# Performance work log

Hardware: AMD Instinct MI355X
Metric: run time of the kernel (lower is better)

## Reference

```python
import jax, jax.numpy as jnp
import numpy as np

B, S, H = 4, 256, 768
NUM_BASIC = 4
NUM_REL = 32            # labels 1..31 are real edges, 0 = no edge
NUM_ALL = 2 * NUM_REL   # bidir: forward slots 0..31, reverse slots 33..63


def setup_inputs() -> dict:
    key = jax.random.key(0)
    k1, k2, k3, k4, k5 = jax.random.split(key, 5)
    hidden_states = jax.random.normal(k1, (B, S, H), dtype=jnp.float32)
    rels = jax.random.randint(k2, (B, S, S), 0, NUM_REL, dtype=jnp.int32)
    # xavier-ish init scale for params
    basic_matrix = jax.random.normal(k3, (NUM_BASIC, H, H), dtype=jnp.float32) * 0.02
    rel_weight = jax.random.normal(k4, (NUM_ALL, NUM_BASIC), dtype=jnp.float32) * 0.1
    self_weight = jax.random.normal(k5, (H, H), dtype=jnp.float32) * 0.02  # Linear weight (out,in)
    return {"hidden_states": hidden_states, "rels": rels,
            "basic_matrix": basic_matrix, "rel_weight": rel_weight,
            "self_weight": self_weight}


def reference(hidden_states, rels, basic_matrix, rel_weight, self_weight):
    dt = hidden_states.dtype
    # forward-direction one-hot relation tensor [B, NUM_ALL, S, S], masked where rels == 0
    fwd_mask = (rels > 0).astype(dt)                                   # [B,S,S]
    fwd_oh = jax.nn.one_hot(rels, NUM_ALL, axis=1, dtype=dt) * fwd_mask[:, None]
    # reverse direction (bidir): labels shifted by NUM_REL, zeroed where no edge
    rev_rels_raw = jnp.transpose(rels, (0, 2, 1))
    rev_rels = jnp.where(rev_rels_raw > 0, rev_rels_raw + NUM_REL, 0)  # {0} U {33..63}
    rev_mask = (rev_rels > 0).astype(dt)
    rev_oh = jax.nn.one_hot(rev_rels, NUM_ALL, axis=1, dtype=dt) * rev_mask[:, None]
    rel_tensor = fwd_oh + rev_oh                                       # [B,R,S,S]

    # basis decomposition: per-relation transform [R, H, H]
    rel_matrix = jnp.einsum('rb,bio->rio', rel_weight, basic_matrix)
    # per-relation transformed hidden states [B,R,S,H]
    r_hidden = jnp.einsum('bsi,rio->brso', hidden_states, rel_matrix)
    # adjacency aggregation [B,R,S,H]
    r_ctx = jnp.einsum('brij,brjo->brio', rel_tensor, r_hidden)
    # mean over neighbors (clamp count at 1)
    num_neighbors = jnp.maximum(rel_tensor.sum(-1), 1.0)               # [B,R,S]
    r_ctx = r_ctx / num_neighbors[..., None]
    context = r_ctx.sum(axis=1)                                        # [B,S,H]
    self_layer = hidden_states @ self_weight.T
    return self_layer + context
```

## Files before the change

### kernel.cpp

```cpp
#include <hip/hip_runtime.h>
#include <stdint.h>

typedef unsigned short u16;
typedef unsigned int u32;
typedef __attribute__((ext_vector_type(8))) short short8;
typedef __attribute__((ext_vector_type(4))) float float4v;

#define Bb 4
#define Ss 256
#define Hh 768
#define NALL 64


__device__ __forceinline__ float b2f(u16 h) {
    u32 u = ((u32)h) << 16;
    float f;
    __builtin_memcpy(&f, &u, 4);
    return f;
}
__device__ __forceinline__ u16 f2b(float f) {
    u32 u;
    __builtin_memcpy(&u, &f, 4);
    u = (u + 0x7fffu + ((u >> 16) & 1u)) >> 16;
    return (u16)u;
}

__global__ __launch_bounds__(256) void k_prep(const float* __restrict__ h,
                                              const int* __restrict__ rels,
                                              const float* __restrict__ basic,
                                              const float* __restrict__ relw,
                                              const float* __restrict__ selfw,
                                              u16* __restrict__ basicT,
                                              u16* __restrict__ coefC,
                                              u16* __restrict__ hbf,
                                              u16* __restrict__ swbf) {
    __shared__ u16 tile[32][34];
    __shared__ float srelw[256];
    __shared__ u32 hist[NALL];
    const int z = blockIdx.x;
    const int t = threadIdx.x;

    if (z < 2304) {
        const int q = z / 576, rem = z % 576;
        const int i0 = (rem % 24) * 32, o0 = (rem / 24) * 32;
        const int tx = t & 31, ty = t >> 5;
        const size_t base = (size_t)q * Hh * Hh;
#pragma unroll
        for (int r = 0; r < 4; ++r)
            tile[ty + 8 * r][tx] = f2b(basic[base + (size_t)(i0 + ty + 8 * r) * Hh + o0 + tx]);
        __syncthreads();
#pragma unroll
        for (int r = 0; r < 4; ++r)
            basicT[base + (size_t)(o0 + ty + 8 * r) * Hh + i0 + tx] = tile[tx][ty + 8 * r];
    } else if (z < 3328) {
        const int r = z - 2304;
        const int i = r & 255, b = r >> 8;
        srelw[t] = relw[t];
        if (t < NALL) hist[t] = 0u;
        __syncthreads();
        const int rfw = rels[(b * Ss + i) * Ss + t];
        const int rcl = rels[(b * Ss + t) * Ss + i];
        if (rfw > 0) atomicAdd(&hist[rfw], 1u);
        if (rcl > 0) atomicAdd(&hist[rcl + 32], 1u);
        __syncthreads();
        float c0 = 0.f, c1 = 0.f, c2 = 0.f, c3 = 0.f;
        if (rfw > 0) {
            const float inv = 1.0f / (float)hist[rfw];
            c0 += srelw[rfw * 4 + 0] * inv; c1 += srelw[rfw * 4 + 1] * inv;
            c2 += srelw[rfw * 4 + 2] * inv; c3 += srelw[rfw * 4 + 3] * inv;
        }
        if (rcl > 0) {
            const int rr = rcl + 32;
            const float inv = 1.0f / (float)hist[rr];
            c0 += srelw[rr * 4 + 0] * inv; c1 += srelw[rr * 4 + 1] * inv;
            c2 += srelw[rr * 4 + 2] * inv; c3 += srelw[rr * 4 + 3] * inv;
        }
        const size_t base = ((size_t)(b * 4) * Ss + i) * Ss + t;
        coefC[base] = f2b(c0);
        coefC[base + (size_t)Ss * Ss] = f2b(c1);
        coefC[base + (size_t)2 * Ss * Ss] = f2b(c2);
        coefC[base + (size_t)3 * Ss * Ss] = f2b(c3);
    } else if (z < 4096) {
        const size_t i = ((size_t)(z - 3328) * 256 + t) * 4;
        const float4 v = *(const float4*)(h + i);
        u32 lo = (u32)f2b(v.x) | ((u32)f2b(v.y) << 16);
        u32 hi = (u32)f2b(v.z) | ((u32)f2b(v.w) << 16);
        *(uint2*)(hbf + i) = make_uint2(lo, hi);
    } else {
        const size_t i = ((size_t)(z - 4096) * 256 + t) * 4;
        const float4 v = *(const float4*)(selfw + i);
        u32 lo = (u32)f2b(v.x) | ((u32)f2b(v.y) << 16);
        u32 hi = (u32)f2b(v.z) | ((u32)f2b(v.w) << 16);
        *(uint2*)(swbf + i) = make_uint2(lo, hi);
    }
}

__global__ __launch_bounds__(256, 4) void k_mid(const u16* __restrict__ basicT,
                                                const u16* __restrict__ hbf,
                                                u16* __restrict__ Gt) {
    __shared__ __align__(16) u16 As[64 * 72];
    __shared__ __align__(16) u16 Bs[64 * 72];
    const int z = blockIdx.x;
    const int o0 = (z % 12) * 64, j0 = ((z / 12) % 4) * 64, bk = z / 48;
    const int b = bk >> 2, q = bk & 3;
    const int t = threadIdx.x;
    const int row = t >> 2, kk = (t & 3) * 16;
    const int w = t >> 6, l = t & 63, quad = l >> 4, l16 = l & 15;

    const u16* aB = basicT + ((size_t)q * Hh + o0 + row) * Hh + kk;
    const u16* bB = hbf + ((size_t)b * Ss + j0 + row) * Hh + kk;

    float4v acc[4];
#pragma unroll
    for (int c = 0; c < 4; ++c) acc[c] = (float4v){0.f, 0.f, 0.f, 0.f};
    uint4 a0 = *(const uint4*)aB, a1 = *(const uint4*)(aB + 8);
    uint4 b0 = *(const uint4*)bB, b1 = *(const uint4*)(bB + 8);

    for (int s = 0; s < 12; ++s) {
        __syncthreads();
        *(uint4*)(&As[row * 72 + kk]) = a0;
        *(uint4*)(&As[row * 72 + kk + 8]) = a1;
        *(uint4*)(&Bs[row * 72 + kk]) = b0;
        *(uint4*)(&Bs[row * 72 + kk + 8]) = b1;
        __syncthreads();
        if (s + 1 < 12) {
            a0 = *(const uint4*)(aB + (s + 1) * 64);
            a1 = *(const uint4*)(aB + (s + 1) * 64 + 8);
            b0 = *(const uint4*)(bB + (s + 1) * 64);
            b1 = *(const uint4*)(bB + (s + 1) * 64 + 8);
        }
#pragma unroll
        for (int k2 = 0; k2 < 64; k2 += 32) {
            const short8 af = *(const short8*)(&As[(16 * w + l16) * 72 + k2 + quad * 8]);
#pragma unroll
            for (int c = 0; c < 4; ++c) {
                const short8 bfr = *(const short8*)(&Bs[(16 * c + l16) * 72 + k2 + quad * 8]);
                acc[c] = __builtin_amdgcn_mfma_f32_16x16x32_bf16(af, bfr, acc[c], 0, 0, 0);
            }
        }
    }

#pragma unroll
    for (int c = 0; c < 4; ++c)
#pragma unroll
        for (int r = 0; r < 4; ++r) {
            const int ol = 16 * w + quad * 4 + r;
            const int jl = 16 * c + l16;
            Gt[((size_t)bk * Hh + o0 + ol) * Ss + j0 + jl] = f2b(acc[c][r]);
        }
}

__global__ __launch_bounds__(256, 4) void k_phase2(const u16* __restrict__ coefC,
                                                   const u16* __restrict__ Gt,
                                                   const u16* __restrict__ hbf,
                                                   const u16* __restrict__ swbf,
                                                   float* __restrict__ out) {
    __shared__ __align__(16) u16 As[64 * 72];
    __shared__ __align__(16) u16 Bs[64 * 72];
    const int z = blockIdx.x;
    const int ot = z % 12, it = (z / 12) % 4, b = z / 48;
    const int t = threadIdx.x;
    const int row = t >> 2, kk = (t & 3) * 16;
    const int w = t >> 6, l = t & 63, quad = l >> 4, l16 = l & 15;

    auto aa = [&](int s) -> const u16* {
        if (s < 16)
            return coefC + ((size_t)(b * 4 + (s >> 2)) * Ss + it * 64 + row) * Ss + (s & 3) * 64 + kk;
        return hbf + ((size_t)b * Ss + it * 64 + row) * Hh + (s - 16) * 64 + kk;
    };
    auto bb = [&](int s) -> const u16* {
        if (s < 16)
            return Gt + ((size_t)(b * 4 + (s >> 2)) * Hh + ot * 64 + row) * Ss + (s & 3) * 64 + kk;
        return swbf + (size_t)(ot * 64 + row) * Hh + (s - 16) * 64 + kk;
    };

    float4v acc[4];
#pragma unroll
    for (int c = 0; c < 4; ++c) acc[c] = (float4v){0.f, 0.f, 0.f, 0.f};
    uint4 a0 = *(const uint4*)aa(0);
    uint4 a1 = *(const uint4*)(aa(0) + 8);
    uint4 b0 = *(const uint4*)bb(0);
    uint4 b1 = *(const uint4*)(bb(0) + 8);

    for (int s = 0; s < 28; ++s) {
        __syncthreads();
        *(uint4*)(&As[row * 72 + kk]) = a0;
        *(uint4*)(&As[row * 72 + kk + 8]) = a1;
        *(uint4*)(&Bs[row * 72 + kk]) = b0;
        *(uint4*)(&Bs[row * 72 + kk + 8]) = b1;
        __syncthreads();
        if (s + 1 < 28) {
            const u16* ap = aa(s + 1);
            const u16* bp = bb(s + 1);
            a0 = *(const uint4*)ap;
            a1 = *(const uint4*)(ap + 8);
            b0 = *(const uint4*)bp;
            b1 = *(const uint4*)(bp + 8);
        }
#pragma unroll
        for (int k2 = 0; k2 < 64; k2 += 32) {
            const short8 af = *(const short8*)(&As[(16 * w + l16) * 72 + k2 + quad * 8]);
#pragma unroll
            for (int c = 0; c < 4; ++c) {
                const short8 bfr = *(const short8*)(&Bs[(16 * c + l16) * 72 + k2 + quad * 8]);
                acc[c] = __builtin_amdgcn_mfma_f32_16x16x32_bf16(af, bfr, acc[c], 0, 0, 0);
            }
        }
    }

#pragma unroll
    for (int c = 0; c < 4; ++c)
#pragma unroll
        for (int r = 0; r < 4; ++r) {
            const int il = 16 * w + quad * 4 + r;
            const int ol = 16 * c + l16;
            out[((size_t)b * Ss + it * 64 + il) * Hh + ot * 64 + ol] = acc[c][r];
        }
}

extern "C" void kernel_launch(void* const* d_in, const int* in_sizes, int n_in,
                              void* d_out, int out_size, void* d_ws, size_t ws_size,
                              hipStream_t stream) {
    const float* h = (const float*)d_in[0];
    const int* rels = (const int*)d_in[1];
    const float* basic = (const float*)d_in[2];
    const float* relw = (const float*)d_in[3];
    const float* selfw = (const float*)d_in[4];
    float* out = (float*)d_out;

    u16* basicT = (u16*)d_ws;
    u16* coefC = basicT + (size_t)4 * Hh * Hh;
    u16* Gt = coefC + (size_t)Bb * 4 * Ss * Ss;
    u16* hbf = Gt + (size_t)Bb * 4 * Hh * Ss;
    u16* swbf = hbf + (size_t)Bb * Ss * Hh;

    k_prep<<<4672, 256, 0, stream>>>(h, rels, basic, relw, selfw, basicT, coefC, hbf, swbf);
    k_mid<<<768, 256, 0, stream>>>(basicT, hbf, Gt);
    k_phase2<<<192, 256, 0, stream>>>(coefC, Gt, hbf, swbf, out);
}
```

Before: 104.2 us.

## Fuse three kernels into one persistent kernel with grid-wide atomic barriers

Replaces the prep, mid-GEMM and final GEMM launches with a single persistent kernel of 512 blocks that loops over work units and synchronises phases with atomic global barriers. Coefficient and self-weight conversion are moved into the same phase as the mid GEMM so they overlap with it. This removes two kernel launch boundaries and their tail effects. It adds spin-wait barrier costs and relies on all blocks being co-resident. The barrier counter reset can race with later blocks on repeated launches, since the magic flag persists between calls.

```diff
diff --git a/kernel.cpp b/kernel.cpp
--- a/kernel.cpp
+++ b/kernel.cpp
@@ -10,6 +10,8 @@
 #define Ss 256
 #define Hh 768
 #define NALL 64
+#define GRID 512
+#define MAGIC 0x1234ABCD
 
 
 __device__ __forceinline__ float b2f(u16 h) {
@@ -25,197 +27,208 @@
     return (u16)u;
 }
 
-__global__ __launch_bounds__(256) void k_prep(const float* __restrict__ h,
-                                              const int* __restrict__ rels,
-                                              const float* __restrict__ basic,
-                                              const float* __restrict__ relw,
-                                              const float* __restrict__ selfw,
-                                              u16* __restrict__ basicT,
-                                              u16* __restrict__ coefC,
-                                              u16* __restrict__ hbf,
-                                              u16* __restrict__ swbf) {
-    __shared__ u16 tile[32][34];
-    __shared__ float srelw[256];
-    __shared__ u32 hist[NALL];
-    const int z = blockIdx.x;
-    const int t = threadIdx.x;
-
-    if (z < 2304) {
-        const int q = z / 576, rem = z % 576;
-        const int i0 = (rem % 24) * 32, o0 = (rem / 24) * 32;
-        const int tx = t & 31, ty = t >> 5;
-        const size_t base = (size_t)q * Hh * Hh;
-#pragma unroll
-        for (int r = 0; r < 4; ++r)
-            tile[ty + 8 * r][tx] = f2b(basic[base + (size_t)(i0 + ty + 8 * r) * Hh + o0 + tx]);
-        __syncthreads();
-#pragma unroll
-        for (int r = 0; r < 4; ++r)
-            basicT[base + (size_t)(o0 + ty + 8 * r) * Hh + i0 + tx] = tile[tx][ty + 8 * r];
-    } else if (z < 3328) {
-        const int r = z - 2304;
-        const int i = r & 255, b = r >> 8;
-        srelw[t] = relw[t];
-        if (t < NALL) hist[t] = 0u;
-        __syncthreads();
-        const int rfw = rels[(b * Ss + i) * Ss + t];
-        const int rcl = rels[(b * Ss + t) * Ss + i];
-        if (rfw > 0) atomicAdd(&hist[rfw], 1u);
-        if (rcl > 0) atomicAdd(&hist[rcl + 32], 1u);
-        __syncthreads();
-        float c0 = 0.f, c1 = 0.f, c2 = 0.f, c3 = 0.f;
-        if (rfw > 0) {
-            const float inv = 1.0f / (float)hist[rfw];
-            c0 += srelw[rfw * 4 + 0] * inv; c1 += srelw[rfw * 4 + 1] * inv;
-            c2 += srelw[rfw * 4 + 2] * inv; c3 += srelw[rfw * 4 + 3] * inv;
-        }
-        if (rcl > 0) {
-            const int rr = rcl + 32;
-            const float inv = 1.0f / (float)hist[rr];
-            c0 += srelw[rr * 4 + 0] * inv; c1 += srelw[rr * 4 + 1] * inv;
-            c2 += srelw[rr * 4 + 2] * inv; c3 += srelw[rr * 4 + 3] * inv;
-        }
-        const size_t base = ((size_t)(b * 4) * Ss + i) * Ss + t;
-        coefC[base] = f2b(c0);
-        coefC[base + (size_t)Ss * Ss] = f2b(c1);
-        coefC[base + (size_t)2 * Ss * Ss] = f2b(c2);
-        coefC[base + (size_t)3 * Ss * Ss] = f2b(c3);
-    } else if (z < 4096) {
-        const size_t i = ((size_t)(z - 3328) * 256 + t) * 4;
-        const float4 v = *(const float4*)(h + i);
-        u32 lo = (u32)f2b(v.x) | ((u32)f2b(v.y) << 16);
-        u32 hi = (u32)f2b(v.z) | ((u32)f2b(v.w) << 16);
-        *(uint2*)(hbf + i) = make_uint2(lo, hi);
-    } else {
-        const size_t i = ((size_t)(z - 4096) * 256 + t) * 4;
-        const float4 v = *(const float4*)(selfw + i);
-        u32 lo = (u32)f2b(v.x) | ((u32)f2b(v.y) << 16);
-        u32 hi = (u32)f2b(v.z) | ((u32)f2b(v.w) << 16);
-        *(uint2*)(swbf + i) = make_uint2(lo, hi);
-    }
-}
-
-__global__ __launch_bounds__(256, 4) void k_mid(const u16* __restrict__ basicT,
-                                                const u16* __restrict__ hbf,
-                                                u16* __restrict__ Gt) {
+__device__ __forceinline__ void gbar(int* bar, int idx) {
+    __syncthreads();
+    if (threadIdx.x == 0) {
+        while (__hip_atomic_load(&bar[0], __ATOMIC_RELAXED, __HIP_MEMORY_SCOPE_AGENT) != MAGIC)
+            __builtin_amdgcn_s_sleep(1);
+        __hip_atomic_fetch_add(&bar[1 + idx], 1, __ATOMIC_RELEASE, __HIP_MEMORY_SCOPE_AGENT);
+        while (__hip_atomic_load(&bar[1 + idx], __ATOMIC_RELAXED, __HIP_MEMORY_SCOPE_AGENT) < GRID)
+            __builtin_amdgcn_s_sleep(2);
+        __builtin_amdgcn_fence(__ATOMIC_ACQUIRE, "agent");
+    }
+    __syncthreads();
+}
+
+__global__ __launch_bounds__(256, 2) void k_fused(const float* __restrict__ h,
+                                                  const int* __restrict__ rels,
+                                                  const float* __restrict__ basic,
+                                                  const float* __restrict__ relw,
+                                                  const float* __restrict__ selfw,
+                                                  u16* __restrict__ basicT,
+                                                  u16* __restrict__ coefC,
+                                                  u16* __restrict__ hbf,
+                                                  u16* __restrict__ swbf,
+                                                  u16* __restrict__ Gt,
+                                                  int* __restrict__ bar,
+                                                  float* __restrict__ out) {
     __shared__ __align__(16) u16 As[64 * 72];
     __shared__ __align__(16) u16 Bs[64 * 72];
-    const int z = blockIdx.x;
-    const int o0 = (z % 12) * 64, j0 = ((z / 12) % 4) * 64, bk = z / 48;
-    const int b = bk >> 2, q = bk & 3;
     const int t = threadIdx.x;
     const int row = t >> 2, kk = (t & 3) * 16;
     const int w = t >> 6, l = t & 63, quad = l >> 4, l16 = l & 15;
 
-    const u16* aB = basicT + ((size_t)q * Hh + o0 + row) * Hh + kk;
-    const u16* bB = hbf + ((size_t)b * Ss + j0 + row) * Hh + kk;
-
-    float4v acc[4];
-#pragma unroll
-    for (int c = 0; c < 4; ++c) acc[c] = (float4v){0.f, 0.f, 0.f, 0.f};
-    uint4 a0 = *(const uint4*)aB, a1 = *(const uint4*)(aB + 8);
-    uint4 b0 = *(const uint4*)bB, b1 = *(const uint4*)(bB + 8);
-
-    for (int s = 0; s < 12; ++s) {
-        __syncthreads();
-        *(uint4*)(&As[row * 72 + kk]) = a0;
-        *(uint4*)(&As[row * 72 + kk + 8]) = a1;
-        *(uint4*)(&Bs[row * 72 + kk]) = b0;
-        *(uint4*)(&Bs[row * 72 + kk + 8]) = b1;
-        __syncthreads();
-        if (s + 1 < 12) {
-            a0 = *(const uint4*)(aB + (s + 1) * 64);
-            a1 = *(const uint4*)(aB + (s + 1) * 64 + 8);
-            b0 = *(const uint4*)(bB + (s + 1) * 64);
-            b1 = *(const uint4*)(bB + (s + 1) * 64 + 8);
+    if (blockIdx.x == 0 && t == 0) {
+        __hip_atomic_store(&bar[1], 0, __ATOMIC_RELAXED, __HIP_MEMORY_SCOPE_AGENT);
+        __hip_atomic_store(&bar[2], 0, __ATOMIC_RELAXED, __HIP_MEMORY_SCOPE_AGENT);
+        __hip_atomic_store(&bar[0], MAGIC, __ATOMIC_RELEASE, __HIP_MEMORY_SCOPE_AGENT);
+    }
+
+    {
+        u16(*tile)[34] = (u16(*)[34])As;
+        for (int u = blockIdx.x; u < 3072; u += GRID) {
+            __syncthreads();
+            if (u < 2304) {
+                const int q = u / 576, rem = u % 576;
+                const int i0 = (rem % 24) * 32, o0 = (rem / 24) * 32;
+                const int tx = t & 31, ty = t >> 5;
+                const size_t base = (size_t)q * Hh * Hh;
+#pragma unroll
+                for (int r = 0; r < 4; ++r)
+                    tile[ty + 8 * r][tx] =
+                        f2b(basic[base + (size_t)(i0 + ty + 8 * r) * Hh + o0 + tx]);
+                __syncthreads();
+#pragma unroll
+                for (int r = 0; r < 4; ++r)
+                    basicT[base + (size_t)(o0 + ty + 8 * r) * Hh + i0 + tx] = tile[tx][ty + 8 * r];
+            } else {
+                const size_t i = ((size_t)(u - 2304) * 256 + t) * 4;
+                const float4 v = *(const float4*)(h + i);
+                u32 lo = (u32)f2b(v.x) | ((u32)f2b(v.y) << 16);
+                u32 hi = (u32)f2b(v.z) | ((u32)f2b(v.w) << 16);
+                *(uint2*)(hbf + i) = make_uint2(lo, hi);
+            }
         }
-#pragma unroll
-        for (int k2 = 0; k2 < 64; k2 += 32) {
-            const short8 af = *(const short8*)(&As[(16 * w + l16) * 72 + k2 + quad * 8]);
-#pragma unroll
-            for (int c = 0; c < 4; ++c) {
-                const short8 bfr = *(const short8*)(&Bs[(16 * c + l16) * 72 + k2 + quad * 8]);
-                acc[c] = __builtin_amdgcn_mfma_f32_16x16x32_bf16(af, bfr, acc[c], 0, 0, 0);
-            }
+    }
+    gbar(bar, 0);
+
+    for (int u = blockIdx.x; u < 2368; u += GRID) {
+        if (u < 768) {
+            const int o0 = (u % 12) * 64, j0 = ((u / 12) % 4) * 64, bk = u / 48;
+            const int b = bk >> 2, q = bk & 3;
+            const u16* aB = basicT + ((size_t)q * Hh + o0 + row) * Hh + kk;
+            const u16* bB = hbf + ((size_t)b * Ss + j0 + row) * Hh + kk;
+            float4v acc[4];
+#pragma unroll
+            for (int c = 0; c < 4; ++c) acc[c] = (float4v){0.f, 0.f, 0.f, 0.f};
+            uint4 a0 = *(const uint4*)aB, a1 = *(const uint4*)(aB + 8);
+            uint4 b0 = *(const uint4*)bB, b1 = *(const uint4*)(bB + 8);
+            for (int s = 0; s < 12; ++s) {
+                __syncthreads();
+                *(uint4*)(&As[row * 72 + kk]) = a0;
+                *(uint4*)(&As[row * 72 + kk + 8]) = a1;
+                *(uint4*)(&Bs[row * 72 + kk]) = b0;
+                *(uint4*)(&Bs[row * 72 + kk + 8]) = b1;
+                __syncthreads();
+                if (s + 1 < 12) {
+                    a0 = *(const uint4*)(aB + (s + 1) * 64);
+                    a1 = *(const uint4*)(aB + (s + 1) * 64 + 8);
+                    b0 = *(const uint4*)(bB + (s + 1) * 64);
+                    b1 = *(const uint4*)(bB + (s + 1) * 64 + 8);
+                }
+#pragma unroll
+                for (int k2 = 0; k2 < 64; k2 += 32) {
+                    const short8 af = *(const short8*)(&As[(16 * w + l16) * 72 + k2 + quad * 8]);
+#pragma unroll
+                    for (int c = 0; c < 4; ++c) {
+                        const short8 bfr = *(const short8*)(&Bs[(16 * c + l16) * 72 + k2 + quad * 8]);
+                        acc[c] = __builtin_amdgcn_mfma_f32_16x16x32_bf16(af, bfr, acc[c], 0, 0, 0);
+                    }
+                }
+            }
+#pragma unroll
+            for (int c = 0; c < 4; ++c)
+#pragma unroll
+                for (int r = 0; r < 4; ++r) {
+                    const int ol = 16 * w + quad * 4 + r;
+                    const int jl = 16 * c + l16;
+                    Gt[((size_t)bk * Hh + o0 + ol) * Ss + j0 + jl] = f2b(acc[c][r]);
+                }
+        } else if (u < 1792) {
+            float* srelw = (float*)As;
+            u32* hist = (u32*)Bs;
+            const int r = u - 768;
+            const int i = r & 255, b = r >> 8;
+            __syncthreads();
+            srelw[t] = relw[t];
+            if (t < NALL) hist[t] = 0u;
+            __syncthreads();
+            const int rfw = rels[(b * Ss + i) * Ss + t];
+            const int rcl = rels[(b * Ss + t) * Ss + i];
+            if (rfw > 0) atomicAdd(&hist[rfw], 1u);
+            if (rcl > 0) atomicAdd(&hist[rcl + 32], 1u);
+            __syncthreads();
+            float c0 = 0.f, c1 = 0.f, c2 = 0.f, c3 = 0.f;
+            if (rfw > 0) {
+                const float inv = 1.0f / (float)hist[rfw];
+                c0 += srelw[rfw * 4 + 0] * inv; c1 += srelw[rfw * 4 + 1] * inv;
+                c2 += srelw[rfw * 4 + 2] * inv; c3 += srelw[rfw * 4 + 3] * inv;
+            }
+            if (rcl > 0) {
+                const int rr = rcl + 32;
+                const float inv = 1.0f / (float)hist[rr];
+                c0 += srelw[rr * 4 + 0] * inv; c1 += srelw[rr * 4 + 1] * inv;
+                c2 += srelw[rr * 4 + 2] * inv; c3 += srelw[rr * 4 + 3] * inv;
+            }
+            const size_t base = ((size_t)(b * 4) * Ss + i) * Ss + t;
+            coefC[base] = f2b(c0);
+            coefC[base + (size_t)Ss * Ss] = f2b(c1);
+            coefC[base + (size_t)2 * Ss * Ss] = f2b(c2);
+            coefC[base + (size_t)3 * Ss * Ss] = f2b(c3);
+        } else {
+            const size_t i = ((size_t)(u - 1792) * 256 + t) * 4;
+            const float4 v = *(const float4*)(selfw + i);
+            u32 lo = (u32)f2b(v.x) | ((u32)f2b(v.y) << 16);
+            u32 hi = (u32)f2b(v.z) | ((u32)f2b(v.w) << 16);
+            *(uint2*)(swbf + i) = make_uint2(lo, hi);
         }
     }
-
-#pragma unroll
-    for (int c = 0; c < 4; ++c)
-#pragma unroll
-        for (int r = 0; r < 4; ++r) {
-            const int ol = 16 * w + quad * 4 + r;
-            const int jl = 16 * c + l16;
-            Gt[((size_t)bk * Hh + o0 + ol) * Ss + j0 + jl] = f2b(acc[c][r]);
+    gbar(bar, 1);
+
+    if (blockIdx.x < 192) {
+        const int z = blockIdx.x;
+        const int ot = z % 12, it = (z / 12) % 4, b = z / 48;
+        auto aa = [&](int s) -> const u16* {
+            if (s < 16)
+                return coefC + ((size_t)(b * 4 + (s >> 2)) * Ss + it * 64 + row) * Ss + (s & 3) * 64 + kk;
+            return hbf + ((size_t)b * Ss + it * 64 + row) * Hh + (s - 16) * 64 + kk;
+        };
+        auto bb = [&](int s) -> const u16* {
+            if (s < 16)
+                return Gt + ((size_t)(b * 4 + (s >> 2)) * Hh + ot * 64 + row) * Ss + (s & 3) * 64 + kk;
+            return swbf + (size_t)(ot * 64 + row) * Hh + (s - 16) * 64 + kk;
+        };
+        float4v acc[4];
+#pragma unroll
+        for (int c = 0; c < 4; ++c) acc[c] = (float4v){0.f, 0.f, 0.f, 0.f};
+        uint4 a0 = *(const uint4*)aa(0);
+        uint4 a1 = *(const uint4*)(aa(0) + 8);
+        uint4 b0 = *(const uint4*)bb(0);
+        uint4 b1 = *(const uint4*)(bb(0) + 8);
+        for (int s = 0; s < 28; ++s) {
+            __syncthreads();
+            *(uint4*)(&As[row * 72 + kk]) = a0;
+            *(uint4*)(&As[row * 72 + kk + 8]) = a1;
+            *(uint4*)(&Bs[row * 72 + kk]) = b0;
+            *(uint4*)(&Bs[row * 72 + kk + 8]) = b1;
+            __syncthreads();
+            if (s + 1 < 28) {
+                const u16* ap = aa(s + 1);
+                const u16* bp = bb(s + 1);
+                a0 = *(const uint4*)ap;
+                a1 = *(const uint4*)(ap + 8);
+                b0 = *(const uint4*)bp;
+                b1 = *(const uint4*)(bp + 8);
+            }
+#pragma unroll
+            for (int k2 = 0; k2 < 64; k2 += 32) {
+                const short8 af = *(const short8*)(&As[(16 * w + l16) * 72 + k2 + quad * 8]);
+#pragma unroll
+                for (int c = 0; c < 4; ++c) {
+                    const short8 bfr = *(const short8*)(&Bs[(16 * c + l16) * 72 + k2 + quad * 8]);
+                    acc[c] = __builtin_amdgcn_mfma_f32_16x16x32_bf16(af, bfr, acc[c], 0, 0, 0);
+                }
+            }
         }
-}
-
-__global__ __launch_bounds__(256, 4) void k_phase2(const u16* __restrict__ coefC,
-                                                   const u16* __restrict__ Gt,
-                                                   const u16* __restrict__ hbf,
-                                                   const u16* __restrict__ swbf,
-                                                   float* __restrict__ out) {
-    __shared__ __align__(16) u16 As[64 * 72];
-    __shared__ __align__(16) u16 Bs[64 * 72];
-    const int z = blockIdx.x;
-    const int ot = z % 12, it = (z / 12) % 4, b = z / 48;
-    const int t = threadIdx.x;
-    const int row = t >> 2, kk = (t & 3) * 16;
-    const int w = t >> 6, l = t & 63, quad = l >> 4, l16 = l & 15;
-
-    auto aa = [&](int s) -> const u16* {
-        if (s < 16)
-            return coefC + ((size_t)(b * 4 + (s >> 2)) * Ss + it * 64 + row) * Ss + (s & 3) * 64 + kk;
-        return hbf + ((size_t)b * Ss + it * 64 + row) * Hh + (s - 16) * 64 + kk;
-    };
-    auto bb = [&](int s) -> const u16* {
-        if (s < 16)
-            return Gt + ((size_t)(b * 4 + (s >> 2)) * Hh + ot * 64 + row) * Ss + (s & 3) * 64 + kk;
-        return swbf + (size_t)(ot * 64 + row) * Hh + (s - 16) * 64 + kk;
-    };
-
-    float4v acc[4];
-#pragma unroll
-    for (int c = 0; c < 4; ++c) acc[c] = (float4v){0.f, 0.f, 0.f, 0.f};
-    uint4 a0 = *(const uint4*)aa(0);
-    uint4 a1 = *(const uint4*)(aa(0) + 8);
-    uint4 b0 = *(const uint4*)bb(0);
-    uint4 b1 = *(const uint4*)(bb(0) + 8);
-
-    for (int s = 0; s < 28; ++s) {
-        __syncthreads();
-        *(uint4*)(&As[row * 72 + kk]) = a0;
-        *(uint4*)(&As[row * 72 + kk + 8]) = a1;
-        *(uint4*)(&Bs[row * 72 + kk]) = b0;
-        *(uint4*)(&Bs[row * 72 + kk + 8]) = b1;
-        __syncthreads();
-        if (s + 1 < 28) {
-            const u16* ap = aa(s + 1);
-            const u16* bp = bb(s + 1);
-            a0 = *(const uint4*)ap;
-            a1 = *(const uint4*)(ap + 8);
-            b0 = *(const uint4*)bp;
-            b1 = *(const uint4*)(bp + 8);
-        }
-#pragma unroll
-        for (int k2 = 0; k2 < 64; k2 += 32) {
-            const short8 af = *(const short8*)(&As[(16 * w + l16) * 72 + k2 + quad * 8]);
-#pragma unroll
-            for (int c = 0; c < 4; ++c) {
-                const short8 bfr = *(const short8*)(&Bs[(16 * c + l16) * 72 + k2 + quad * 8]);
-                acc[c] = __builtin_amdgcn_mfma_f32_16x16x32_bf16(af, bfr, acc[c], 0, 0, 0);
-            }
-        }
-    }
-
-#pragma unroll
-    for (int c = 0; c < 4; ++c)
-#pragma unroll
-        for (int r = 0; r < 4; ++r) {
-            const int il = 16 * w + quad * 4 + r;
-            const int ol = 16 * c + l16;
-            out[((size_t)b * Ss + it * 64 + il) * Hh + ot * 64 + ol] = acc[c][r];
-        }
+#pragma unroll
+        for (int c = 0; c < 4; ++c)
+#pragma unroll
+            for (int r = 0; r < 4; ++r) {
+                const int il = 16 * w + quad * 4 + r;
+                const int ol = 16 * c + l16;
+                out[((size_t)b * Ss + it * 64 + il) * Hh + ot * 64 + ol] = acc[c][r];
+            }
+    }
 }
 
 extern "C" void kernel_launch(void* const* d_in, const int* in_sizes, int n_in,
@@ -233,8 +246,8 @@
     u16* Gt = coefC + (size_t)Bb * 4 * Ss * Ss;
     u16* hbf = Gt + (size_t)Bb * 4 * Hh * Ss;
     u16* swbf = hbf + (size_t)Bb * Ss * Hh;
-
-    k_prep<<<4672, 256, 0, stream>>>(h, rels, basic, relw, selfw, basicT, coefC, hbf, swbf);
-    k_mid<<<768, 256, 0, stream>>>(basicT, hbf, Gt);
-    k_phase2<<<192, 256, 0, stream>>>(coefC, Gt, hbf, swbf, out);
-}
+    int* bar = (int*)(swbf + (size_t)Hh * Hh);
+
+    k_fused<<<GRID, 256, 0, stream>>>(h, rels, basic, relw, selfw,
+                                      basicT, coefC, hbf, swbf, Gt, bar, out);
+}
```

Result: slower. 197.8 us (+89.9%).

## Fuse mid and output GEMMs into one persistent kernel with grid barrier

Applied to the files above, without the earlier changes.

Merges the G = basis·h GEMM and the final coefficient/self-weight GEMM into a single 1024-block kernel. The two phases are separated by an atomic-counter grid barrier, and the output phase runs on every fifth block. The separate bf16 conversion of hidden states and self weight is dropped; fp32 values are loaded and converted while staging into shared memory. This removes one launch and one conversion pass. In exchange it adds barrier spin overhead and wider fp32 loads, and it relies on all 1024 blocks being co-resident. The barrier's reset of its own counters has a possible cross-launch race.

```diff
diff --git a/kernel.cpp b/kernel.cpp
--- a/kernel.cpp
+++ b/kernel.cpp
@@ -10,30 +10,36 @@
 #define Ss 256
 #define Hh 768
 #define NALL 64
-
-
-__device__ __forceinline__ float b2f(u16 h) {
-    u32 u = ((u32)h) << 16;
-    float f;
-    __builtin_memcpy(&f, &u, 4);
-    return f;
-}
+#define GRID2 1024
+#define MAGIC 0x1234ABCD
+
+
 __device__ __forceinline__ u16 f2b(float f) {
     u32 u;
     __builtin_memcpy(&u, &f, 4);
     u = (u + 0x7fffu + ((u >> 16) & 1u)) >> 16;
     return (u16)u;
 }
-
-__global__ __launch_bounds__(256) void k_prep(const float* __restrict__ h,
-                                              const int* __restrict__ rels,
-                                              const float* __restrict__ basic,
-                                              const float* __restrict__ relw,
-                                              const float* __restrict__ selfw,
-                                              u16* __restrict__ basicT,
-                                              u16* __restrict__ coefC,
-                                              u16* __restrict__ hbf,
-                                              u16* __restrict__ swbf) {
+union pk8 { uint4 v; u16 e[8]; };
+__device__ __forceinline__ uint4 cvt8(float4 f0, float4 f1) {
+    pk8 r;
+    r.e[0] = f2b(f0.x); r.e[1] = f2b(f0.y); r.e[2] = f2b(f0.z); r.e[3] = f2b(f0.w);
+    r.e[4] = f2b(f1.x); r.e[5] = f2b(f1.y); r.e[6] = f2b(f1.z); r.e[7] = f2b(f1.w);
+    return r.v;
+}
+
+__device__ __forceinline__ void poll_eq(int* p, int val) {
+    if (__hip_atomic_load(p, __ATOMIC_RELAXED, __HIP_MEMORY_SCOPE_AGENT) == val) return;
+    __builtin_amdgcn_s_sleep(2);
+    while (__hip_atomic_load(p, __ATOMIC_RELAXED, __HIP_MEMORY_SCOPE_AGENT) != val)
+        __builtin_amdgcn_s_sleep(16);
+}
+
+__global__ __launch_bounds__(256) void k_prep2(const int* __restrict__ rels,
+                                               const float* __restrict__ basic,
+                                               const float* __restrict__ relw,
+                                               u16* __restrict__ basicT,
+                                               u16* __restrict__ coefC) {
     __shared__ u16 tile[32][34];
     __shared__ float srelw[256];
     __shared__ u32 hist[NALL];
@@ -52,7 +58,7 @@
 #pragma unroll
         for (int r = 0; r < 4; ++r)
             basicT[base + (size_t)(o0 + ty + 8 * r) * Hh + i0 + tx] = tile[tx][ty + 8 * r];
-    } else if (z < 3328) {
+    } else {
         const int r = z - 2304;
         const int i = r & 255, b = r >> 8;
         srelw[t] = relw[t];
@@ -80,142 +86,152 @@
         coefC[base + (size_t)Ss * Ss] = f2b(c1);
         coefC[base + (size_t)2 * Ss * Ss] = f2b(c2);
         coefC[base + (size_t)3 * Ss * Ss] = f2b(c3);
-    } else if (z < 4096) {
-        const size_t i = ((size_t)(z - 3328) * 256 + t) * 4;
-        const float4 v = *(const float4*)(h + i);
-        u32 lo = (u32)f2b(v.x) | ((u32)f2b(v.y) << 16);
-        u32 hi = (u32)f2b(v.z) | ((u32)f2b(v.w) << 16);
-        *(uint2*)(hbf + i) = make_uint2(lo, hi);
-    } else {
-        const size_t i = ((size_t)(z - 4096) * 256 + t) * 4;
-        const float4 v = *(const float4*)(selfw + i);
-        u32 lo = (u32)f2b(v.x) | ((u32)f2b(v.y) << 16);
-        u32 hi = (u32)f2b(v.z) | ((u32)f2b(v.w) << 16);
-        *(uint2*)(swbf + i) = make_uint2(lo, hi);
-    }
-}
-
-__global__ __launch_bounds__(256, 4) void k_mid(const u16* __restrict__ basicT,
-                                                const u16* __restrict__ hbf,
-                                                u16* __restrict__ Gt) {
+    }
+}
+
+__global__ __launch_bounds__(256, 4) void k_fused2(const float* __restrict__ h,
+                                                   const float* __restrict__ selfw,
+                                                   const u16* __restrict__ basicT,
+                                                   const u16* __restrict__ coefC,
+                                                   u16* __restrict__ Gt,
+                                                   int* __restrict__ bar,
+                                                   float* __restrict__ out) {
     __shared__ __align__(16) u16 As[64 * 72];
     __shared__ __align__(16) u16 Bs[64 * 72];
-    const int z = blockIdx.x;
-    const int o0 = (z % 12) * 64, j0 = ((z / 12) % 4) * 64, bk = z / 48;
-    const int b = bk >> 2, q = bk & 3;
     const int t = threadIdx.x;
     const int row = t >> 2, kk = (t & 3) * 16;
     const int w = t >> 6, l = t & 63, quad = l >> 4, l16 = l & 15;
 
-    const u16* aB = basicT + ((size_t)q * Hh + o0 + row) * Hh + kk;
-    const u16* bB = hbf + ((size_t)b * Ss + j0 + row) * Hh + kk;
-
-    float4v acc[4];
-#pragma unroll
-    for (int c = 0; c < 4; ++c) acc[c] = (float4v){0.f, 0.f, 0.f, 0.f};
-    uint4 a0 = *(const uint4*)aB, a1 = *(const uint4*)(aB + 8);
-    uint4 b0 = *(const uint4*)bB, b1 = *(const uint4*)(bB + 8);
-
-    for (int s = 0; s < 12; ++s) {
-        __syncthreads();
-        *(uint4*)(&As[row * 72 + kk]) = a0;
-        *(uint4*)(&As[row * 72 + kk + 8]) = a1;
-        *(uint4*)(&Bs[row * 72 + kk]) = b0;
-        *(uint4*)(&Bs[row * 72 + kk + 8]) = b1;
-        __syncthreads();
-        if (s + 1 < 12) {
-            a0 = *(const uint4*)(aB + (s + 1) * 64);
-            a1 = *(const uint4*)(aB + (s + 1) * 64 + 8);
-            b0 = *(const uint4*)(bB + (s + 1) * 64);
-            b1 = *(const uint4*)(bB + (s + 1) * 64 + 8);
-        }
-#pragma unroll
-        for (int k2 = 0; k2 < 64; k2 += 32) {
-            const short8 af = *(const short8*)(&As[(16 * w + l16) * 72 + k2 + quad * 8]);
-#pragma unroll
-            for (int c = 0; c < 4; ++c) {
-                const short8 bfr = *(const short8*)(&Bs[(16 * c + l16) * 72 + k2 + quad * 8]);
-                acc[c] = __builtin_amdgcn_mfma_f32_16x16x32_bf16(af, bfr, acc[c], 0, 0, 0);
-            }
-        }
-    }
-
-#pragma unroll
-    for (int c = 0; c < 4; ++c)
-#pragma unroll
-        for (int r = 0; r < 4; ++r) {
-            const int ol = 16 * w + quad * 4 + r;
-            const int jl = 16 * c + l16;
-            Gt[((size_t)bk * Hh + o0 + ol) * Ss + j0 + jl] = f2b(acc[c][r]);
-        }
-}
-
-__global__ __launch_bounds__(256, 4) void k_phase2(const u16* __restrict__ coefC,
-                                                   const u16* __restrict__ Gt,
-                                                   const u16* __restrict__ hbf,
-                                                   const u16* __restrict__ swbf,
-                                                   float* __restrict__ out) {
-    __shared__ __align__(16) u16 As[64 * 72];
-    __shared__ __align__(16) u16 Bs[64 * 72];
-    const int z = blockIdx.x;
-    const int ot = z % 12, it = (z / 12) % 4, b = z / 48;
-    const int t = threadIdx.x;
-    const int row = t >> 2, kk = (t & 3) * 16;
-    const int w = t >> 6, l = t & 63, quad = l >> 4, l16 = l & 15;
-
-    auto aa = [&](int s) -> const u16* {
-        if (s < 16)
-            return coefC + ((size_t)(b * 4 + (s >> 2)) * Ss + it * 64 + row) * Ss + (s & 3) * 64 + kk;
-        return hbf + ((size_t)b * Ss + it * 64 + row) * Hh + (s - 16) * 64 + kk;
-    };
-    auto bb = [&](int s) -> const u16* {
-        if (s < 16)
-            return Gt + ((size_t)(b * 4 + (s >> 2)) * Hh + ot * 64 + row) * Ss + (s & 3) * 64 + kk;
-        return swbf + (size_t)(ot * 64 + row) * Hh + (s - 16) * 64 + kk;
-    };
-
-    float4v acc[4];
-#pragma unroll
-    for (int c = 0; c < 4; ++c) acc[c] = (float4v){0.f, 0.f, 0.f, 0.f};
-    uint4 a0 = *(const uint4*)aa(0);
-    uint4 a1 = *(const uint4*)(aa(0) + 8);
-    uint4 b0 = *(const uint4*)bb(0);
-    uint4 b1 = *(const uint4*)(bb(0) + 8);
-
-    for (int s = 0; s < 28; ++s) {
-        __syncthreads();
-        *(uint4*)(&As[row * 72 + kk]) = a0;
-        *(uint4*)(&As[row * 72 + kk + 8]) = a1;
-        *(uint4*)(&Bs[row * 72 + kk]) = b0;
-        *(uint4*)(&Bs[row * 72 + kk + 8]) = b1;
-        __syncthreads();
-        if (s + 1 < 28) {
-            const u16* ap = aa(s + 1);
-            const u16* bp = bb(s + 1);
-            a0 = *(const uint4*)ap;
-            a1 = *(const uint4*)(ap + 8);
-            b0 = *(const uint4*)bp;
-            b1 = *(const uint4*)(bp + 8);
-        }
-#pragma unroll
-        for (int k2 = 0; k2 < 64; k2 += 32) {
-            const short8 af = *(const short8*)(&As[(16 * w + l16) * 72 + k2 + quad * 8]);
-#pragma unroll
-            for (int c = 0; c < 4; ++c) {
-                const short8 bfr = *(const short8*)(&Bs[(16 * c + l16) * 72 + k2 + quad * 8]);
-                acc[c] = __builtin_amdgcn_mfma_f32_16x16x32_bf16(af, bfr, acc[c], 0, 0, 0);
-            }
-        }
-    }
-
-#pragma unroll
-    for (int c = 0; c < 4; ++c)
-#pragma unroll
-        for (int r = 0; r < 4; ++r) {
-            const int il = 16 * w + quad * 4 + r;
-            const int ol = 16 * c + l16;
-            out[((size_t)b * Ss + it * 64 + il) * Hh + ot * 64 + ol] = acc[c][r];
-        }
+    if (blockIdx.x == 0 && t == 0) {
+        __hip_atomic_store(&bar[32], 0, __ATOMIC_RELAXED, __HIP_MEMORY_SCOPE_AGENT);
+        __hip_atomic_store(&bar[64], 0, __ATOMIC_RELAXED, __HIP_MEMORY_SCOPE_AGENT);
+        __hip_atomic_store(&bar[0], MAGIC, __ATOMIC_RELEASE, __HIP_MEMORY_SCOPE_AGENT);
+    }
+
+    if (blockIdx.x < 768) {
+        const int u = blockIdx.x;
+        const int o0 = (u % 12) * 64, j0 = ((u / 12) % 4) * 64, bk = u / 48;
+        const int b = bk >> 2, q = bk & 3;
+        const u16* aB = basicT + ((size_t)q * Hh + o0 + row) * Hh + kk;
+        const float* bB = h + ((size_t)b * Ss + j0 + row) * Hh + kk;
+        float4v acc[4];
+#pragma unroll
+        for (int c = 0; c < 4; ++c) acc[c] = (float4v){0.f, 0.f, 0.f, 0.f};
+        uint4 a0 = *(const uint4*)aB, a1 = *(const uint4*)(aB + 8);
+        float4 f0 = *(const float4*)bB, f1 = *(const float4*)(bB + 4);
+        float4 f2 = *(const float4*)(bB + 8), f3 = *(const float4*)(bB + 12);
+        for (int s = 0; s < 12; ++s) {
+            __syncthreads();
+            *(uint4*)(&As[row * 72 + kk]) = a0;
+            *(uint4*)(&As[row * 72 + kk + 8]) = a1;
+            *(uint4*)(&Bs[row * 72 + kk]) = cvt8(f0, f1);
+            *(uint4*)(&Bs[row * 72 + kk + 8]) = cvt8(f2, f3);
+            __syncthreads();
+            if (s + 1 < 12) {
+                a0 = *(const uint4*)(aB + (s + 1) * 64);
+                a1 = *(const uint4*)(aB + (s + 1) * 64 + 8);
+                const float* bp = bB + (s + 1) * 64;
+                f0 = *(const float4*)bp;      f1 = *(const float4*)(bp + 4);
+                f2 = *(const float4*)(bp + 8); f3 = *(const float4*)(bp + 12);
+            }
+#pragma unroll
+            for (int k2 = 0; k2 < 64; k2 += 32) {
+                const short8 af = *(const short8*)(&As[(16 * w + l16) * 72 + k2 + quad * 8]);
+#pragma unroll
+                for (int c = 0; c < 4; ++c) {
+                    const short8 bfr = *(const short8*)(&Bs[(16 * c + l16) * 72 + k2 + quad * 8]);
+                    acc[c] = __builtin_amdgcn_mfma_f32_16x16x32_bf16(af, bfr, acc[c], 0, 0, 0);
+                }
+            }
+        }
+#pragma unroll
+        for (int c = 0; c < 4; ++c)
+#pragma unroll
+            for (int r = 0; r < 4; ++r) {
+                const int ol = 16 * w + quad * 4 + r;
+                const int jl = 16 * c + l16;
+                Gt[((size_t)bk * Hh + o0 + ol) * Ss + j0 + jl] = f2b(acc[c][r]);
+            }
+    }
+
+    __syncthreads();
+    if (t == 0) {
+        poll_eq(&bar[0], MAGIC);
+        const int old = __hip_atomic_fetch_add(&bar[32], 1, __ATOMIC_RELEASE, __HIP_MEMORY_SCOPE_AGENT);
+        if (old == GRID2 - 1)
+            __hip_atomic_store(&bar[64], MAGIC, __ATOMIC_RELEASE, __HIP_MEMORY_SCOPE_AGENT);
+        poll_eq(&bar[64], MAGIC);
+        __builtin_amdgcn_fence(__ATOMIC_ACQUIRE, "agent");
+    }
+    __syncthreads();
+
+    if (blockIdx.x % 5 == 0 && blockIdx.x / 5 < 192) {
+        const int z = blockIdx.x / 5;
+        const int ot = z % 12, it = (z / 12) % 4, b = z / 48;
+        uint4 ua0, ua1, ub0, ub1;
+        float4 fa0, fa1, fa2, fa3, fb0, fb1, fb2, fb3;
+        bool af32 = false, bf32 = false;
+        auto loadA = [&](int s) {
+            if (s < 16) {
+                const u16* p = coefC + ((size_t)(b * 4 + (s >> 2)) * Ss + it * 64 + row) * Ss + (s & 3) * 64 + kk;
+                ua0 = *(const uint4*)p; ua1 = *(const uint4*)(p + 8); af32 = false;
+            } else {
+                const float* p = h + ((size_t)b * Ss + it * 64 + row) * Hh + (s - 16) * 64 + kk;
+                fa0 = *(const float4*)p;      fa1 = *(const float4*)(p + 4);
+                fa2 = *(const float4*)(p + 8); fa3 = *(const float4*)(p + 12); af32 = true;
+            }
+        };
+        auto loadB = [&](int s) {
+            if (s < 16) {
+                const u16* p = Gt + ((size_t)(b * 4 + (s >> 2)) * Hh + ot * 64 + row) * Ss + (s & 3) * 64 + kk;
+                ub0 = *(const uint4*)p; ub1 = *(const uint4*)(p + 8); bf32 = false;
+            } else {
+                const float* p = selfw + (size_t)(ot * 64 + row) * Hh + (s - 16) * 64 + kk;
+                fb0 = *(const float4*)p;      fb1 = *(const float4*)(p + 4);
+                fb2 = *(const float4*)(p + 8); fb3 = *(const float4*)(p + 12); bf32 = true;
+            }
+        };
+        float4v acc[4];
+#pragma unroll
+        for (int c = 0; c < 4; ++c) acc[c] = (float4v){0.f, 0.f, 0.f, 0.f};
+        loadA(0); loadB(0);
+        for (int s = 0; s < 28; ++s) {
+            __syncthreads();
+            if (af32) {
+                *(uint4*)(&As[row * 72 + kk]) = cvt8(fa0, fa1);
+                *(uint4*)(&As[row * 72 + kk + 8]) = cvt8(fa2, fa3);
+            } else {
+                *(uint4*)(&As[row * 72 + kk]) = ua0;
+                *(uint4*)(&As[row * 72 + kk + 8]) = ua1;
+            }
+            if (bf32) {
+                *(uint4*)(&Bs[row * 72 + kk]) = cvt8(fb0, fb1);
+                *(uint4*)(&Bs[row * 72 + kk + 8]) = cvt8(fb2, fb3);
+            } else {
+                *(uint4*)(&Bs[row * 72 + kk]) = ub0;
+                *(uint4*)(&Bs[row * 72 + kk + 8]) = ub1;
+            }
+            __syncthreads();
+            if (s + 1 < 28) { loadA(s + 1); loadB(s + 1); }
+#pragma unroll
+            for (int k2 = 0; k2 < 64; k2 += 32) {
+                const short8 af = *(const short8*)(&As[(16 * w + l16) * 72 + k2 + quad * 8]);
+#pragma unroll
+                for (int c = 0; c < 4; ++c) {
+                    const short8 bfr = *(const short8*)(&Bs[(16 * c + l16) * 72 + k2 + quad * 8]);
+                    acc[c] = __builtin_amdgcn_mfma_f32_16x16x32_bf16(af, bfr, acc[c], 0, 0, 0);
+                }
+            }
+        }
+#pragma unroll
+        for (int c = 0; c < 4; ++c)
+#pragma unroll
+            for (int r = 0; r < 4; ++r) {
+                const int il = 16 * w + quad * 4 + r;
+                const int ol = 16 * c + l16;
+                out[((size_t)b * Ss + it * 64 + il) * Hh + ot * 64 + ol] = acc[c][r];
+            }
+    }
 }
 
 extern "C" void kernel_launch(void* const* d_in, const int* in_sizes, int n_in,
@@ -231,10 +247,8 @@
     u16* basicT = (u16*)d_ws;
     u16* coefC = basicT + (size_t)4 * Hh * Hh;
     u16* Gt = coefC + (size_t)Bb * 4 * Ss * Ss;
-    u16* hbf = Gt + (size_t)Bb * 4 * Hh * Ss;
-    u16* swbf = hbf + (size_t)Bb * Ss * Hh;
-
-    k_prep<<<4672, 256, 0, stream>>>(h, rels, basic, relw, selfw, basicT, coefC, hbf, swbf);
-    k_mid<<<768, 256, 0, stream>>>(basicT, hbf, Gt);
-    k_phase2<<<192, 256, 0, stream>>>(coefC, Gt, hbf, swbf, out);
-}
+    int* bar = (int*)(Gt + (size_t)Bb * 4 * Hh * Ss);
+
+    k_prep2<<<3328, 256, 0, stream>>>(rels, basic, relw, basicT, coefC);
+    k_fused2<<<GRID2, 256, 0, stream>>>(h, selfw, basicT, coefC, Gt, bar, out);
+}
```

Result: slower. 165.0 us (+58.4%).
